# Optimization experiments

Measured on AMD Instinct MI355X. Metric: run time of the kernel, lower is better.

Reference implementation:

```python
import jax, jax.numpy as jnp
import numpy as np

TEMPERATURE = 0.07
NEG_INF = -1e30


def setup_inputs() -> dict:
    key = jax.random.key(0)
    k_h, k_m, k_l, k_w = jax.random.split(key, 4)
    B, L, H, P = 32, 1024, 1280, 128
    hidden_states = jax.random.normal(k_h, (B, L, H), dtype=jnp.float32)
    attention_mask = jax.random.randint(k_m, (B, L), 0, 2).astype(jnp.int32)
    labels = jax.random.randint(k_l, (B, L), 0, 4).astype(jnp.int32)
    proj_w = jax.random.normal(k_w, (H, P), dtype=jnp.float32) * 0.02
    proj_b = jnp.zeros((P,), dtype=jnp.float32)
    return {
        "hidden_states": hidden_states,
        "proj_w": proj_w,
        "proj_b": proj_b,
        "attention_mask": attention_mask,
        "labels": labels,
    }


def reference(hidden_states, proj_w, proj_b, attention_mask, labels):
    # Projection head (dropout is inactive at eval) + L2 normalize
    emb = hidden_states @ proj_w + proj_b                     # [B, L, P]
    emb = emb / jnp.linalg.norm(emb, axis=-1, keepdims=True)

    B, L, _ = emb.shape
    attn_valid = attention_mask.astype(bool)                  # [B, L]
    valid = attn_valid & (labels != -100)                     # anchor/candidate validity

    # Per-sequence token-token similarity, temperature-scaled
    sim = jnp.einsum("bip,bjp->bij", emb, emb) / TEMPERATURE  # [B, L, L]

    eye = jnp.eye(L, dtype=bool)                              # [L, L]
    col_valid = valid[:, None, :]                             # valid candidate j
    # Row max over valid columns (includes self, as in original filtered emb)
    m = jax.lax.stop_gradient(
        jnp.max(jnp.where(col_valid, sim, NEG_INF), axis=2, keepdims=True)
    )
    logits = sim - m
    logits_mask = col_valid & ~eye[None]                      # exclude self, invalid cols
    exp_logits = jnp.where(logits_mask, jnp.exp(logits), 0.0)
    log_prob = logits - jnp.log(exp_logits.sum(axis=2, keepdims=True) + 1e-12)

    # Positives: same label, same sequence, not self, both valid
    same_label = labels[:, :, None] == labels[:, None, :]
    pos_mask = (same_label & logits_mask & valid[:, :, None]).astype(sim.dtype)

    sum_pos_log_prob = (pos_mask * log_prob).sum(axis=2)      # [B, L]
    anchor_loss = sum_pos_log_prob / (pos_mask.sum(axis=2) + 1e-12)

    valid_f = valid.astype(sim.dtype)
    n_anchor = jnp.maximum(valid_f.sum(axis=1), 1.0)
    loss_seq = -(valid_f * anchor_loss).sum(axis=1) / n_anchor  # mean over valid anchors

    # Sequence included iff attention_mask has >= 2 valid tokens (original check)
    seq_ok = (attention_mask.sum(axis=1) >= 2)
    n_seq = jnp.maximum(seq_ok.sum().astype(sim.dtype), 1.0)
    loss = jnp.where(seq_ok, loss_seq, 0.0).sum() / n_seq
    return loss
```

## Files before the change

kernel.cpp:

```cpp
#include <hip/hip_runtime.h>
#include <hip/hip_bf16.h>
#include <cstddef>
#include <cstdint>

#define NB   32
#define LSEQ 1024
#define HDIM 1280
#define PDIM 128
#define KCHUNKS 40

typedef unsigned short ushort_t;
typedef __bf16 bf16x8 __attribute__((ext_vector_type(8)));
typedef float  f32x4  __attribute__((ext_vector_type(4)));

#define WT_OFF  256
#define E_OFF   (256 + HDIM * PDIM * 2)

__device__ __forceinline__ ushort_t bf16_rne(float x) {
  unsigned u = __float_as_uint(x);
  unsigned r = u + 0x7fffu + ((u >> 16) & 1u);
  return (ushort_t)(r >> 16);
}

__global__ __launch_bounds__(256) void k0_wt(const float* __restrict__ pw,
                                             ushort_t* __restrict__ wB,
                                             float* __restrict__ wsf) {
  if (blockIdx.x == 0 && threadIdx.x < 64) wsf[threadIdx.x] = 0.0f;
  const int idx = blockIdx.x * 256 + threadIdx.x;
  const int k = idx >> 7, n = idx & 127;
  const int kc = k >> 5, kr = k & 31;
  const int t = n >> 4, lm = n & 15;
  const int lq = kr >> 3, j = kr & 7;
  const int l = lq * 16 + lm;
  wB[((size_t)(kc * 8 + t) * 64 + l) * 8 + j] = bf16_rne(pw[(size_t)k * PDIM + n]);
}

__global__ __launch_bounds__(64, 2) void k1_mfma(const float* __restrict__ hs,
                                                 const ushort_t* __restrict__ wB,
                                                 const float* __restrict__ pb,
                                                 ushort_t* __restrict__ e) {
  const int l = threadIdx.x;
  const int lm = l & 15, lq = l >> 4;
  const int m0 = blockIdx.x * 16;

  const float*    arow  = hs + (size_t)(m0 + lm) * HDIM + lq * 8;
  const ushort_t* bbase = wB + (size_t)l * 8;

  float4 Abuf[4][2];
#pragma unroll
  for (int d = 0; d < 4; ++d) {
    Abuf[d][0] = *(const float4*)(arow + d * 32);
    Abuf[d][1] = *(const float4*)(arow + d * 32 + 4);
  }
  bf16x8 Bc[8], Bn[8], Bm[8];
#pragma unroll
  for (int t = 0; t < 8; ++t) {
    Bc[t] = *(const bf16x8*)(bbase + (size_t)(0 * 8 + t) * 512);
    Bn[t] = *(const bf16x8*)(bbase + (size_t)(1 * 8 + t) * 512);
  }

  f32x4 acc[8];
#pragma unroll
  for (int t = 0; t < 8; ++t) acc[t] = (f32x4){0.f, 0.f, 0.f, 0.f};

#pragma unroll 4
  for (int kc = 0; kc < KCHUNKS; ++kc) {
    const int kb = (kc + 2 < KCHUNKS) ? kc + 2 : KCHUNKS - 1;
#pragma unroll
    for (int t = 0; t < 8; ++t)
      Bm[t] = *(const bf16x8*)(bbase + (size_t)(kb * 8 + t) * 512);

    union { ushort_t u[8]; bf16x8 v; } cv;
    const float4 f0 = Abuf[kc & 3][0];
    const float4 f1 = Abuf[kc & 3][1];
    cv.u[0] = bf16_rne(f0.x); cv.u[1] = bf16_rne(f0.y);
    cv.u[2] = bf16_rne(f0.z); cv.u[3] = bf16_rne(f0.w);
    cv.u[4] = bf16_rne(f1.x); cv.u[5] = bf16_rne(f1.y);
    cv.u[6] = bf16_rne(f1.z); cv.u[7] = bf16_rne(f1.w);
    const bf16x8 a = cv.v;

    const int ka = (kc + 4 < KCHUNKS) ? kc + 4 : KCHUNKS - 1;
    Abuf[kc & 3][0] = *(const float4*)(arow + ka * 32);
    Abuf[kc & 3][1] = *(const float4*)(arow + ka * 32 + 4);

#pragma unroll
    for (int t = 0; t < 8; ++t)
      acc[t] = __builtin_amdgcn_mfma_f32_16x16x32_bf16(a, Bc[t], acc[t], 0, 0, 0);

#pragma unroll
    for (int t = 0; t < 8; ++t) { Bc[t] = Bn[t]; Bn[t] = Bm[t]; }
  }

  float pbv[8];
#pragma unroll
  for (int t = 0; t < 8; ++t) pbv[t] = pb[t * 16 + lm];

#pragma unroll
  for (int r = 0; r < 4; ++r) {
    float v[8];
    float s2 = 0.f;
#pragma unroll
    for (int t = 0; t < 8; ++t) {
      v[t] = acc[t][r] + pbv[t];
      s2 = fmaf(v[t], v[t], s2);
    }
    s2 += __shfl_xor(s2, 1, 64);
    s2 += __shfl_xor(s2, 2, 64);
    s2 += __shfl_xor(s2, 4, 64);
    s2 += __shfl_xor(s2, 8, 64);
    const float inv = 1.0f / sqrtf(s2);
    ushort_t* erow = e + (size_t)(m0 + lq * 4 + r) * PDIM + lm;
#pragma unroll
    for (int t = 0; t < 8; ++t) erow[t * 16] = bf16_rne(v[t] * inv);
  }
}

__global__ __launch_bounds__(256, 3) void k2_loss(const ushort_t* __restrict__ e,
                                                  const int* __restrict__ mask,
                                                  const int* __restrict__ labels,
                                                  float* __restrict__ accb) {
  __shared__ float part[4][32][3];

  const int tid = threadIdx.x;
  const int l = tid & 63, w = tid >> 6;
  const int b  = blockIdx.x >> 5;
  const int i0 = (blockIdx.x & 31) << 5;
  const int lm = l & 15, lq = l >> 4;

  const ushort_t* eb   = e + (size_t)b * LSEQ * PDIM;
  const int*      mrow = mask + b * LSEQ;
  const int*      lrow = labels + b * LSEQ;

  bf16x8 af[2][4];
#pragma unroll
  for (int ii = 0; ii < 2; ++ii) {
    const ushort_t* aptr = eb + (size_t)(i0 + ii * 16 + lm) * PDIM + lq * 8;
#pragma unroll
    for (int c = 0; c < 4; ++c) af[ii][c] = *(const bf16x8*)(aptr + c * 32);
  }

  int  li[2][4], ar[2][4];
  bool vi[2][4];
#pragma unroll
  for (int ii = 0; ii < 2; ++ii)
#pragma unroll
    for (int r = 0; r < 4; ++r) {
      ar[ii][r] = i0 + ii * 16 + lq * 4 + r;
      li[ii][r] = lrow[ar[ii][r]];
      vi[ii][r] = (mrow[ar[ii][r]] != 0) && (li[ii][r] != -100);
    }

  float d[2][4] = {}, ps[2][4] = {}, pc[2][4] = {};
  const float invT = 1.0f / 0.07f;

  int jt = w * 16;
  bf16x8 Bc[4];
  int ljc, mjc;
  {
    const int j = jt * 16 + lm;
    const ushort_t* bptr = eb + (size_t)j * PDIM + lq * 8;
#pragma unroll
    for (int c = 0; c < 4; ++c) Bc[c] = *(const bf16x8*)(bptr + c * 32);
    ljc = lrow[j];
    mjc = mrow[j];
  }

#pragma unroll 1
  for (int s = 0; s < 16; ++s, ++jt) {
    bf16x8 Bn[4];
    int ljn = 0, mjn = 0;
    if (s < 15) {
      const int jn = (jt + 1) * 16 + lm;
      const ushort_t* bptr = eb + (size_t)jn * PDIM + lq * 8;
#pragma unroll
      for (int c = 0; c < 4; ++c) Bn[c] = *(const bf16x8*)(bptr + c * 32);
      ljn = lrow[jn];
      mjn = mrow[jn];
    }

    const int j = jt * 16 + lm;
    const bool cvj = (mjc != 0) && (ljc != -100);
#pragma unroll
    for (int ii = 0; ii < 2; ++ii) {
      f32x4 acc = (f32x4){0.f, 0.f, 0.f, 0.f};
#pragma unroll
      for (int c = 0; c < 4; ++c)
        acc = __builtin_amdgcn_mfma_f32_16x16x32_bf16(af[ii][c], Bc[c], acc, 0, 0, 0);
#pragma unroll
      for (int r = 0; r < 4; ++r) {
        const float sv = acc[r] * invT;
        const bool dm  = cvj && (j != ar[ii][r]);
        const float ex = __expf(sv);
        d[ii][r] += dm ? ex : 0.f;
        const bool pos = dm && (ljc == li[ii][r]) && vi[ii][r];
        ps[ii][r] += pos ? sv : 0.f;
        pc[ii][r] += pos ? 1.f : 0.f;
      }
    }

#pragma unroll
    for (int c = 0; c < 4; ++c) Bc[c] = Bn[c];
    ljc = ljn; mjc = mjn;
  }

#pragma unroll
  for (int ii = 0; ii < 2; ++ii)
#pragma unroll
    for (int r = 0; r < 4; ++r) {
#pragma unroll
      for (int off = 1; off < 16; off <<= 1) {
        d[ii][r]  += __shfl_xor(d[ii][r], off, 64);
        ps[ii][r] += __shfl_xor(ps[ii][r], off, 64);
        pc[ii][r] += __shfl_xor(pc[ii][r], off, 64);
      }
    }
  if (lm == 0) {
#pragma unroll
    for (int ii = 0; ii < 2; ++ii)
#pragma unroll
      for (int r = 0; r < 4; ++r) {
        part[w][ii * 16 + lq * 4 + r][0] = d[ii][r];
        part[w][ii * 16 + lq * 4 + r][1] = ps[ii][r];
        part[w][ii * 16 + lq * 4 + r][2] = pc[ii][r];
      }
  }
  __syncthreads();

  if (tid < 32) {
    float D = 0.f, P = 0.f, C = 0.f;
#pragma unroll
    for (int w2 = 0; w2 < 4; ++w2) {
      D += part[w2][tid][0];
      P += part[w2][tid][1];
      C += part[w2][tid][2];
    }
    const float logD = logf(D + 1e-12f);
    float al = (P - C * logD) / (C + 1e-12f);
#pragma unroll
    for (int off = 1; off < 32; off <<= 1) al += __shfl_xor(al, off, 64);
    if (tid == 0) atomicAdd(&accb[b], al);
  }
}

__global__ __launch_bounds__(1024) void k3_final(const int* __restrict__ mask,
                                                 const int* __restrict__ labels,
                                                 const float* __restrict__ accb,
                                                 float* __restrict__ out) {
  __shared__ float lossv[NB];
  __shared__ float okv[NB];
  const int t = threadIdx.x;
  const int b = t >> 5, sub = t & 31;

  int cm = 0, cv = 0;
#pragma unroll
  for (int q = 0; q < 8; ++q) {
    const int idx = b * LSEQ + q * 128 + sub * 4;
    const int4 mv = *(const int4*)(mask + idx);
    const int4 lv = *(const int4*)(labels + idx);
    cm += mv.x + mv.y + mv.z + mv.w;
    cv += ((mv.x != 0 && lv.x != -100) ? 1 : 0) +
          ((mv.y != 0 && lv.y != -100) ? 1 : 0) +
          ((mv.z != 0 && lv.z != -100) ? 1 : 0) +
          ((mv.w != 0 && lv.w != -100) ? 1 : 0);
  }
#pragma unroll
  for (int off = 16; off; off >>= 1) {
    cm += __shfl_xor(cm, off, 64);
    cv += __shfl_xor(cv, off, 64);
  }
  if (sub == 0) {
    const bool ok = (cm >= 2);
    lossv[b] = ok ? (-accb[b] / fmaxf((float)cv, 1.0f)) : 0.0f;
    okv[b]   = ok ? 1.0f : 0.0f;
  }
  __syncthreads();
  if (t < NB) {
    float lv = lossv[t], ov = okv[t];
#pragma unroll
    for (int off = 16; off; off >>= 1) {
      lv += __shfl_xor(lv, off, 64);
      ov += __shfl_xor(ov, off, 64);
    }
    if (t == 0) out[0] = lv / fmaxf(ov, 1.0f);
  }
}

extern "C" void kernel_launch(void* const* d_in, const int* in_sizes, int n_in,
                              void* d_out, int out_size, void* d_ws, size_t ws_size,
                              hipStream_t stream) {
  (void)in_sizes; (void)n_in; (void)out_size; (void)ws_size;
  const float* hs     = (const float*)d_in[0];
  const float* pw     = (const float*)d_in[1];
  const float* pb     = (const float*)d_in[2];
  const int*   mask   = (const int*)d_in[3];
  const int*   labels = (const int*)d_in[4];
  float* out = (float*)d_out;

  char* wsb = (char*)d_ws;
  float*    wsf  = (float*)wsb;
  float*    accb = wsf;
  ushort_t* wB   = (ushort_t*)(wsb + WT_OFF);
  ushort_t* e    = (ushort_t*)(wsb + E_OFF);

  k0_wt<<<(HDIM * PDIM) / 256, 256, 0, stream>>>(pw, wB, wsf);
  k1_mfma<<<(NB * LSEQ) / 16, 64, 0, stream>>>(hs, wB, pb, e);
  k2_loss<<<NB * 32, 256, 0, stream>>>(e, mask, labels, accb);
  k3_final<<<1, 1024, 0, stream>>>(mask, labels, accb, out);
}
```

Measured before the change: 314.8 us.

## Restructure projection GEMM into 32-row tiles with async LDS double-buffering

The projection kernel moves from one-wave blocks of 16 rows to four-wave blocks of 32 rows. Each wave computes a 32-column slice of the output and reads its B fragments directly from global memory. The fp32 activations are staged into LDS with global_load_lds and double buffered, so they are shared across waves instead of each wave loading its own. Row norms are now combined across waves through shared memory, which adds syncs and LDS traffic. The aim is better occupancy and less redundant activation loading in this memory-bound GEMM.

```diff
diff --git a/kernel.cpp b/kernel.cpp
--- a/kernel.cpp
+++ b/kernel.cpp
@@ -7,7 +7,7 @@
 #define LSEQ 1024
 #define HDIM 1280
 #define PDIM 128
-#define KCHUNKS 40
+#define KSTEPS 20
 
 typedef unsigned short ushort_t;
 typedef __bf16 bf16x8 __attribute__((ext_vector_type(8)));
@@ -21,6 +21,11 @@
   unsigned r = u + 0x7fffu + ((u >> 16) & 1u);
   return (ushort_t)(r >> 16);
 }
+
+#define GLD_LDS16(gp, lp)                                                      \
+  __builtin_amdgcn_global_load_lds(                                            \
+      (const __attribute__((address_space(1))) void*)(gp),                     \
+      (__attribute__((address_space(3))) void*)(lp), 16, 0, 0)
 
 __global__ __launch_bounds__(256) void k0_wt(const float* __restrict__ pw,
                                              ushort_t* __restrict__ wB,
@@ -35,84 +40,126 @@
   wB[((size_t)(kc * 8 + t) * 64 + l) * 8 + j] = bf16_rne(pw[(size_t)k * PDIM + n]);
 }
 
-__global__ __launch_bounds__(64, 2) void k1_mfma(const float* __restrict__ hs,
-                                                 const ushort_t* __restrict__ wB,
-                                                 const float* __restrict__ pb,
-                                                 ushort_t* __restrict__ e) {
-  const int l = threadIdx.x;
+__global__ __launch_bounds__(256, 4) void k1_mfma(const float* __restrict__ hs,
+                                                  const ushort_t* __restrict__ wB,
+                                                  const float* __restrict__ pb,
+                                                  ushort_t* __restrict__ e) {
+  __shared__ __align__(16) char smem[2][8192];
+
+  const int tid = threadIdx.x;
+  const int l = tid & 63, w = tid >> 6;
   const int lm = l & 15, lq = l >> 4;
-  const int m0 = blockIdx.x * 16;
-
-  const float*    arow  = hs + (size_t)(m0 + lm) * HDIM + lq * 8;
-  const ushort_t* bbase = wB + (size_t)l * 8;
-
-  float4 Abuf[4][2];
-#pragma unroll
-  for (int d = 0; d < 4; ++d) {
-    Abuf[d][0] = *(const float4*)(arow + d * 32);
-    Abuf[d][1] = *(const float4*)(arow + d * 32 + 4);
-  }
-  bf16x8 Bc[8], Bn[8], Bm[8];
-#pragma unroll
-  for (int t = 0; t < 8; ++t) {
-    Bc[t] = *(const bf16x8*)(bbase + (size_t)(0 * 8 + t) * 512);
-    Bn[t] = *(const bf16x8*)(bbase + (size_t)(1 * 8 + t) * 512);
-  }
-
-  f32x4 acc[8];
-#pragma unroll
-  for (int t = 0; t < 8; ++t) acc[t] = (f32x4){0.f, 0.f, 0.f, 0.f};
-
-#pragma unroll 4
-  for (int kc = 0; kc < KCHUNKS; ++kc) {
-    const int kb = (kc + 2 < KCHUNKS) ? kc + 2 : KCHUNKS - 1;
-#pragma unroll
-    for (int t = 0; t < 8; ++t)
-      Bm[t] = *(const bf16x8*)(bbase + (size_t)(kb * 8 + t) * 512);
-
-    union { ushort_t u[8]; bf16x8 v; } cv;
-    const float4 f0 = Abuf[kc & 3][0];
-    const float4 f1 = Abuf[kc & 3][1];
-    cv.u[0] = bf16_rne(f0.x); cv.u[1] = bf16_rne(f0.y);
-    cv.u[2] = bf16_rne(f0.z); cv.u[3] = bf16_rne(f0.w);
-    cv.u[4] = bf16_rne(f1.x); cv.u[5] = bf16_rne(f1.y);
-    cv.u[6] = bf16_rne(f1.z); cv.u[7] = bf16_rne(f1.w);
-    const bf16x8 a = cv.v;
-
-    const int ka = (kc + 4 < KCHUNKS) ? kc + 4 : KCHUNKS - 1;
-    Abuf[kc & 3][0] = *(const float4*)(arow + ka * 32);
-    Abuf[kc & 3][1] = *(const float4*)(arow + ka * 32 + 4);
-
-#pragma unroll
-    for (int t = 0; t < 8; ++t)
-      acc[t] = __builtin_amdgcn_mfma_f32_16x16x32_bf16(a, Bc[t], acc[t], 0, 0, 0);
-
-#pragma unroll
-    for (int t = 0; t < 8; ++t) { Bc[t] = Bn[t]; Bn[t] = Bm[t]; }
-  }
-
-  float pbv[8];
-#pragma unroll
-  for (int t = 0; t < 8; ++t) pbv[t] = pb[t * 16 + lm];
-
-#pragma unroll
-  for (int r = 0; r < 4; ++r) {
-    float v[8];
-    float s2 = 0.f;
-#pragma unroll
-    for (int t = 0; t < 8; ++t) {
-      v[t] = acc[t][r] + pbv[t];
-      s2 = fmaf(v[t], v[t], s2);
-    }
-    s2 += __shfl_xor(s2, 1, 64);
-    s2 += __shfl_xor(s2, 2, 64);
-    s2 += __shfl_xor(s2, 4, 64);
-    s2 += __shfl_xor(s2, 8, 64);
-    const float inv = 1.0f / sqrtf(s2);
-    ushort_t* erow = e + (size_t)(m0 + lq * 4 + r) * PDIM + lm;
-#pragma unroll
-    for (int t = 0; t < 8; ++t) erow[t * 16] = bf16_rne(v[t] * inv);
-  }
+  const int m0 = blockIdx.x * 32;
+
+  const int o0 = w * 1024 + l * 16;
+  const int o1 = o0 + 4096;
+  const float* ga0;
+  const float* ga1;
+  {
+    int p = o0 >> 10;
+    int row = ((p >> 2) << 4) + lm;
+    int kk  = (((p >> 1) & 1) << 5) + (lq << 3) + ((p & 1) << 2);
+    ga0 = hs + (size_t)(m0 + row) * HDIM + kk;
+    p = o1 >> 10;
+    row = ((p >> 2) << 4) + lm;
+    kk  = (((p >> 1) & 1) << 5) + (lq << 3) + ((p & 1) << 2);
+    ga1 = hs + (size_t)(m0 + row) * HDIM + kk;
+  }
+  const ushort_t* bB = wB + (size_t)(w * 2) * 512 + (size_t)l * 8;
+
+  f32x4 acc[2][2];
+#pragma unroll
+  for (int m = 0; m < 2; ++m)
+#pragma unroll
+    for (int tt = 0; tt < 2; ++tt) acc[m][tt] = (f32x4){0.f, 0.f, 0.f, 0.f};
+
+  GLD_LDS16(ga0, &smem[0][o0]);
+  GLD_LDS16(ga1, &smem[0][o1]);
+  ga0 += 64; ga1 += 64;
+  __syncthreads();
+
+#pragma unroll 2
+  for (int st = 0; st < KSTEPS; ++st) {
+    const int cur = st & 1;
+
+    bf16x8 Bf[2][2];
+#pragma unroll
+    for (int kh = 0; kh < 2; ++kh)
+#pragma unroll
+      for (int tt = 0; tt < 2; ++tt)
+        Bf[tt][kh] =
+            *(const bf16x8*)(bB + (size_t)(st * 2 + kh) * 4096 + tt * 512);
+
+    if (st < KSTEPS - 1) {
+      GLD_LDS16(ga0, &smem[cur ^ 1][o0]);
+      GLD_LDS16(ga1, &smem[cur ^ 1][o1]);
+      ga0 += 64; ga1 += 64;
+    }
+
+    bf16x8 a[2][2];
+#pragma unroll
+    for (int m = 0; m < 2; ++m)
+#pragma unroll
+      for (int kh = 0; kh < 2; ++kh) {
+        const f32x4 f0 =
+            *(const f32x4*)&smem[cur][(m * 4 + kh * 2 + 0) * 1024 + l * 16];
+        const f32x4 f1 =
+            *(const f32x4*)&smem[cur][(m * 4 + kh * 2 + 1) * 1024 + l * 16];
+        union { ushort_t u[8]; bf16x8 v; } cv;
+        cv.u[0] = bf16_rne(f0[0]); cv.u[1] = bf16_rne(f0[1]);
+        cv.u[2] = bf16_rne(f0[2]); cv.u[3] = bf16_rne(f0[3]);
+        cv.u[4] = bf16_rne(f1[0]); cv.u[5] = bf16_rne(f1[1]);
+        cv.u[6] = bf16_rne(f1[2]); cv.u[7] = bf16_rne(f1[3]);
+        a[m][kh] = cv.v;
+      }
+
+#pragma unroll
+    for (int m = 0; m < 2; ++m)
+#pragma unroll
+      for (int tt = 0; tt < 2; ++tt)
+#pragma unroll
+        for (int kh = 0; kh < 2; ++kh)
+          acc[m][tt] = __builtin_amdgcn_mfma_f32_16x16x32_bf16(
+              a[m][kh], Bf[tt][kh], acc[m][tt], 0, 0, 0);
+
+    __syncthreads();
+  }
+
+  const float pbv0 = pb[w * 32 + lm];
+  const float pbv1 = pb[w * 32 + 16 + lm];
+#pragma unroll
+  for (int m = 0; m < 2; ++m)
+#pragma unroll
+    for (int r = 0; r < 4; ++r) {
+      acc[m][0][r] += pbv0;
+      acc[m][1][r] += pbv1;
+    }
+
+  float* sp = (float*)smem;
+#pragma unroll
+  for (int m = 0; m < 2; ++m)
+#pragma unroll
+    for (int r = 0; r < 4; ++r) {
+      float s2 = acc[m][0][r] * acc[m][0][r] + acc[m][1][r] * acc[m][1][r];
+      s2 += __shfl_xor(s2, 1, 64);
+      s2 += __shfl_xor(s2, 2, 64);
+      s2 += __shfl_xor(s2, 4, 64);
+      s2 += __shfl_xor(s2, 8, 64);
+      if (lm == 0) sp[w * 32 + m * 16 + lq * 4 + r] = s2;
+    }
+  __syncthreads();
+
+#pragma unroll
+  for (int m = 0; m < 2; ++m)
+#pragma unroll
+    for (int r = 0; r < 4; ++r) {
+      const int row = m * 16 + lq * 4 + r;
+      const float tot = sp[row] + sp[32 + row] + sp[64 + row] + sp[96 + row];
+      const float inv = 1.0f / sqrtf(tot);
+      ushort_t* er = e + (size_t)(m0 + row) * PDIM + w * 32 + lm;
+      er[0]  = bf16_rne(acc[m][0][r] * inv);
+      er[16] = bf16_rne(acc[m][1][r] * inv);
+    }
 }
 
 __global__ __launch_bounds__(256, 3) void k2_loss(const ushort_t* __restrict__ e,
@@ -303,7 +350,7 @@
   ushort_t* e    = (ushort_t*)(wsb + E_OFF);
 
   k0_wt<<<(HDIM * PDIM) / 256, 256, 0, stream>>>(pw, wB, wsf);
-  k1_mfma<<<(NB * LSEQ) / 16, 64, 0, stream>>>(hs, wB, pb, e);
+  k1_mfma<<<(NB * LSEQ) / 32, 256, 0, stream>>>(hs, wB, pb, e);
   k2_loss<<<NB * 32, 256, 0, stream>>>(e, mask, labels, accb);
   k3_final<<<1, 1024, 0, stream>>>(mask, labels, accb, out);
 }
```

Measured after the change: 299.8 us. 4.7% less time.

## Split projection GEMM K dimension across four waves with LDS reduction

Applied to the files above, without the earlier changes.

The projection kernel now launches 256 threads per 16-row tile instead of one wave. Each wave handles a quarter of the hidden dimension (320), and the partial accumulators are summed through shared memory before bias, L2 normalisation and bf16 store. This raises the number of waves in flight and shortens each wave's serial MFMA chain, which targets latency in the memory-bound read of the fp32 hidden states. In exchange it adds LDS traffic, a block barrier, and per-block shared memory that may limit occupancy.

```diff
diff --git a/kernel.cpp b/kernel.cpp
--- a/kernel.cpp
+++ b/kernel.cpp
@@ -7,7 +7,6 @@
 #define LSEQ 1024
 #define HDIM 1280
 #define PDIM 128
-#define KCHUNKS 40
 
 typedef unsigned short ushort_t;
 typedef __bf16 bf16x8 __attribute__((ext_vector_type(8)));
@@ -35,84 +34,81 @@
   wB[((size_t)(kc * 8 + t) * 64 + l) * 8 + j] = bf16_rne(pw[(size_t)k * PDIM + n]);
 }
 
-__global__ __launch_bounds__(64, 2) void k1_mfma(const float* __restrict__ hs,
-                                                 const ushort_t* __restrict__ wB,
-                                                 const float* __restrict__ pb,
-                                                 ushort_t* __restrict__ e) {
-  const int l = threadIdx.x;
+__global__ __launch_bounds__(256, 4) void k1_mfma(const float* __restrict__ hs,
+                                                  const ushort_t* __restrict__ wB,
+                                                  const float* __restrict__ pb,
+                                                  ushort_t* __restrict__ e) {
+  __shared__ float sp[4 * 16 * 132];
+
+  const int tid = threadIdx.x;
+  const int l = tid & 63, w = tid >> 6;
   const int lm = l & 15, lq = l >> 4;
   const int m0 = blockIdx.x * 16;
 
-  const float*    arow  = hs + (size_t)(m0 + lm) * HDIM + lq * 8;
-  const ushort_t* bbase = wB + (size_t)l * 8;
-
-  float4 Abuf[4][2];
-#pragma unroll
-  for (int d = 0; d < 4; ++d) {
-    Abuf[d][0] = *(const float4*)(arow + d * 32);
-    Abuf[d][1] = *(const float4*)(arow + d * 32 + 4);
-  }
-  bf16x8 Bc[8], Bn[8], Bm[8];
+  const float* arow = hs + (size_t)(m0 + lm) * HDIM + w * 320 + lq * 8;
+  const ushort_t* bB = wB + (size_t)w * 40960 + (size_t)l * 8;
+
+  f32x4 acc[8];
+#pragma unroll
+  for (int t = 0; t < 8; ++t) acc[t] = (f32x4){0.f, 0.f, 0.f, 0.f};
+
+  f32x4 Ag0[10], Ag1[10];
+  Ag0[0] = *(const f32x4*)(arow + 0);
+  Ag1[0] = *(const f32x4*)(arow + 4);
+  Ag0[1] = *(const f32x4*)(arow + 32);
+  Ag1[1] = *(const f32x4*)(arow + 36);
+
+#pragma unroll
+  for (int c = 0; c < 10; ++c) {
+    bf16x8 Bf[8];
+#pragma unroll
+    for (int t = 0; t < 8; ++t)
+      Bf[t] = *(const bf16x8*)(bB + (size_t)c * 4096 + t * 512);
+
+    if (c + 2 < 10) {
+      Ag0[c + 2] = *(const f32x4*)(arow + (c + 2) * 32);
+      Ag1[c + 2] = *(const f32x4*)(arow + (c + 2) * 32 + 4);
+    }
+
+    const f32x4 f0 = Ag0[c], f1 = Ag1[c];
+    union { ushort_t u[8]; bf16x8 v; } cv;
+    cv.u[0] = bf16_rne(f0[0]); cv.u[1] = bf16_rne(f0[1]);
+    cv.u[2] = bf16_rne(f0[2]); cv.u[3] = bf16_rne(f0[3]);
+    cv.u[4] = bf16_rne(f1[0]); cv.u[5] = bf16_rne(f1[1]);
+    cv.u[6] = bf16_rne(f1[2]); cv.u[7] = bf16_rne(f1[3]);
+    const bf16x8 a = cv.v;
+
+#pragma unroll
+    for (int t = 0; t < 8; ++t)
+      acc[t] = __builtin_amdgcn_mfma_f32_16x16x32_bf16(a, Bf[t], acc[t], 0, 0, 0);
+  }
+
+#pragma unroll
+  for (int t = 0; t < 8; ++t)
+#pragma unroll
+    for (int r = 0; r < 4; ++r)
+      sp[(w * 16 + lq * 4 + r) * 132 + t * 16 + lm] = acc[t][r];
+  __syncthreads();
+
+  const int row = w * 4 + lq;
+  float val[8];
+  float s2 = 0.f;
 #pragma unroll
   for (int t = 0; t < 8; ++t) {
-    Bc[t] = *(const bf16x8*)(bbase + (size_t)(0 * 8 + t) * 512);
-    Bn[t] = *(const bf16x8*)(bbase + (size_t)(1 * 8 + t) * 512);
-  }
-
-  f32x4 acc[8];
-#pragma unroll
-  for (int t = 0; t < 8; ++t) acc[t] = (f32x4){0.f, 0.f, 0.f, 0.f};
-
-#pragma unroll 4
-  for (int kc = 0; kc < KCHUNKS; ++kc) {
-    const int kb = (kc + 2 < KCHUNKS) ? kc + 2 : KCHUNKS - 1;
-#pragma unroll
-    for (int t = 0; t < 8; ++t)
-      Bm[t] = *(const bf16x8*)(bbase + (size_t)(kb * 8 + t) * 512);
-
-    union { ushort_t u[8]; bf16x8 v; } cv;
-    const float4 f0 = Abuf[kc & 3][0];
-    const float4 f1 = Abuf[kc & 3][1];
-    cv.u[0] = bf16_rne(f0.x); cv.u[1] = bf16_rne(f0.y);
-    cv.u[2] = bf16_rne(f0.z); cv.u[3] = bf16_rne(f0.w);
-    cv.u[4] = bf16_rne(f1.x); cv.u[5] = bf16_rne(f1.y);
-    cv.u[6] = bf16_rne(f1.z); cv.u[7] = bf16_rne(f1.w);
-    const bf16x8 a = cv.v;
-
-    const int ka = (kc + 4 < KCHUNKS) ? kc + 4 : KCHUNKS - 1;
-    Abuf[kc & 3][0] = *(const float4*)(arow + ka * 32);
-    Abuf[kc & 3][1] = *(const float4*)(arow + ka * 32 + 4);
-
-#pragma unroll
-    for (int t = 0; t < 8; ++t)
-      acc[t] = __builtin_amdgcn_mfma_f32_16x16x32_bf16(a, Bc[t], acc[t], 0, 0, 0);
-
-#pragma unroll
-    for (int t = 0; t < 8; ++t) { Bc[t] = Bn[t]; Bn[t] = Bm[t]; }
-  }
-
-  float pbv[8];
-#pragma unroll
-  for (int t = 0; t < 8; ++t) pbv[t] = pb[t * 16 + lm];
-
-#pragma unroll
-  for (int r = 0; r < 4; ++r) {
-    float v[8];
-    float s2 = 0.f;
-#pragma unroll
-    for (int t = 0; t < 8; ++t) {
-      v[t] = acc[t][r] + pbv[t];
-      s2 = fmaf(v[t], v[t], s2);
-    }
-    s2 += __shfl_xor(s2, 1, 64);
-    s2 += __shfl_xor(s2, 2, 64);
-    s2 += __shfl_xor(s2, 4, 64);
-    s2 += __shfl_xor(s2, 8, 64);
-    const float inv = 1.0f / sqrtf(s2);
-    ushort_t* erow = e + (size_t)(m0 + lq * 4 + r) * PDIM + lm;
-#pragma unroll
-    for (int t = 0; t < 8; ++t) erow[t * 16] = bf16_rne(v[t] * inv);
-  }
+    const int col = t * 16 + lm;
+    val[t] = sp[(0 * 16 + row) * 132 + col] + sp[(1 * 16 + row) * 132 + col] +
+             sp[(2 * 16 + row) * 132 + col] + sp[(3 * 16 + row) * 132 + col] +
+             pb[col];
+    s2 = fmaf(val[t], val[t], s2);
+  }
+  s2 += __shfl_xor(s2, 1, 64);
+  s2 += __shfl_xor(s2, 2, 64);
+  s2 += __shfl_xor(s2, 4, 64);
+  s2 += __shfl_xor(s2, 8, 64);
+  const float inv = 1.0f / sqrtf(s2);
+  ushort_t* er = e + (size_t)(m0 + row) * PDIM + lm;
+#pragma unroll
+  for (int t = 0; t < 8; ++t) er[t * 16] = bf16_rne(val[t] * inv);
 }
 
 __global__ __launch_bounds__(256, 3) void k2_loss(const ushort_t* __restrict__ e,
@@ -303,7 +299,7 @@
   ushort_t* e    = (ushort_t*)(wsb + E_OFF);
 
   k0_wt<<<(HDIM * PDIM) / 256, 256, 0, stream>>>(pw, wB, wsf);
-  k1_mfma<<<(NB * LSEQ) / 16, 64, 0, stream>>>(hs, wB, pb, e);
+  k1_mfma<<<(NB * LSEQ) / 16, 256, 0, stream>>>(hs, wB, pb, e);
   k2_loss<<<NB * 32, 256, 0, stream>>>(e, mask, labels, accb);
   k3_final<<<1, 1024, 0, stream>>>(mask, labels, accb, out);
 }
```

After: 317.1 us. About the same (+0.7%).
